# Optimization experiments

Hardware: AMD Instinct MI355X
Metric: run time of the kernel (lower is better)

Reference implementation:

```python
import jax, jax.numpy as jnp
import numpy as np

POOL_D, POOL_H, POOL_W = 4, 7, 7
SPATIAL_SCALE = 0.25
SAMPLING_RATIO = 2


def setup_inputs() -> dict:
    key = jax.random.key(0)
    k1, k2, k3, k4 = jax.random.split(key, 4)
    N, C, D, H, W = 2, 128, 32, 64, 64
    features = jax.random.normal(k1, (N, C, D, H, W), dtype=jnp.float32)
    R = 256
    inv = 1.0 / SPATIAL_SCALE  # rois live in image coords; features at stride 4
    batch = jax.random.randint(k2, (R,), 0, N).astype(jnp.float32)
    dims = jnp.array([D, H, W], dtype=jnp.float32)
    starts = jax.random.uniform(k3, (R, 3)) * dims * inv * 0.6
    sizes = (0.1 + 0.3 * jax.random.uniform(k4, (R, 3))) * dims * inv
    z1, y1, x1 = starts[:, 0], starts[:, 1], starts[:, 2]
    z2, y2, x2 = z1 + sizes[:, 0], y1 + sizes[:, 1], x1 + sizes[:, 2]
    # roi layout: (batch_idx, x1, y1, z1, x2, y2, z2)
    rois = jnp.stack([batch, x1, y1, z1, x2, y2, z2], axis=1).astype(jnp.float32)
    return {"features": features, "rois": rois}


def _axis(coords, size):
    # classic RoIAlign border handling: outside [-1, size] -> 0 contribution
    valid = (coords >= -1.0) & (coords <= float(size))
    c = jnp.clip(coords, 0.0, float(size) - 1.0)
    lo = jnp.floor(c)
    hi = jnp.minimum(lo + 1.0, float(size) - 1.0)
    w = c - lo  # weight of the hi corner
    return lo.astype(jnp.int32), hi.astype(jnp.int32), w, valid


def roi_align_3d(features, rois):
    N, C, D, H, W = features.shape
    R = rois.shape[0]
    sr = SAMPLING_RATIO
    b = rois[:, 0].astype(jnp.int32)
    x1 = rois[:, 1] * SPATIAL_SCALE
    y1 = rois[:, 2] * SPATIAL_SCALE
    z1 = rois[:, 3] * SPATIAL_SCALE
    x2 = rois[:, 4] * SPATIAL_SCALE
    y2 = rois[:, 5] * SPATIAL_SCALE
    z2 = rois[:, 6] * SPATIAL_SCALE
    rd = jnp.maximum(z2 - z1, 1.0)
    rh = jnp.maximum(y2 - y1, 1.0)
    rw = jnp.maximum(x2 - x1, 1.0)

    def sample_coords(start, extent, P):
        # sampling_ratio sample centers per output bin -> [R, P*sr]
        t = (jnp.arange(P * sr, dtype=jnp.float32) + 0.5) / sr
        return start[:, None] + t[None, :] * (extent / P)[:, None]

    zs = sample_coords(z1, rd, POOL_D)  # [R, SD]
    ys = sample_coords(y1, rh, POOL_H)  # [R, SH]
    xs = sample_coords(x1, rw, POOL_W)  # [R, SW]
    zlo, zhi, wz, vz = _axis(zs, D)
    ylo, yhi, wy, vy = _axis(ys, H)
    xlo, xhi, wx, vx = _axis(xs, W)

    B = b[:, None, None, None]
    Z = lambda a: a[:, :, None, None]
    Y = lambda a: a[:, None, :, None]
    X = lambda a: a[:, None, None, :]

    def g(zi, yi, xi):
        # gather -> [R, SD, SH, SW, C]
        return features[B, :, Z(zi), Y(yi), X(xi)]

    wz1, wy1, wx1 = Z(wz)[..., None], Y(wy)[..., None], X(wx)[..., None]
    wz0, wy0, wx0 = 1.0 - wz1, 1.0 - wy1, 1.0 - wx1
    val = (g(zlo, ylo, xlo) * (wz0 * wy0 * wx0)
           + g(zlo, ylo, xhi) * (wz0 * wy0 * wx1)
           + g(zlo, yhi, xlo) * (wz0 * wy1 * wx0)
           + g(zlo, yhi, xhi) * (wz0 * wy1 * wx1)
           + g(zhi, ylo, xlo) * (wz1 * wy0 * wx0)
           + g(zhi, ylo, xhi) * (wz1 * wy0 * wx1)
           + g(zhi, yhi, xlo) * (wz1 * wy1 * wx0)
           + g(zhi, yhi, xhi) * (wz1 * wy1 * wx1))
    valid = (Z(vz) & Y(vy) & X(vx))[..., None]
    val = jnp.where(valid, val, 0.0)
    # average the sr^3 samples per bin
    val = val.reshape(R, POOL_D, sr, POOL_H, sr, POOL_W, sr, C)
    out = val.mean(axis=(2, 4, 6))  # [R, PD, PH, PW, C]
    return jnp.transpose(out, (0, 4, 1, 2, 3))  # [R, C, PD, PH, PW]


def reference(features, rois):
    return roi_align_3d(features, rois)
```

## Files before the change

kernel.cpp:

```cpp
#include <hip/hip_runtime.h>

constexpr int C_  = 128;
constexpr int D_  = 32;
constexpr int H_  = 64;
constexpr int W_  = 64;
constexpr int PD = 4;
constexpr int PH = 7;
constexpr int PW = 7;
constexpr int SR = 2;
constexpr float SCALE = 0.25f;
constexpr int S_ = D_ * H_ * W_;
constexpr int BINS_PER_ROI = PD * PH * PW;
constexpr int SLAB = PH * PW;

typedef float vf4 __attribute__((ext_vector_type(4)));

__device__ __forceinline__ void axis2(float start, float extent, int P, int p,
                                      int size, int lo[2], int hi[2],
                                      float w[2], bool v[2]) {
    float bin = extent / (float)P;
#pragma unroll
    for (int u = 0; u < 2; ++u) {
        float t = ((float)(p * SR + u) + 0.5f) / (float)SR;
        float coord = start + t * bin;
        v[u] = (coord >= -1.0f) && (coord <= (float)size);
        float cc = fminf(fmaxf(coord, 0.0f), (float)size - 1.0f);
        float fl = floorf(cc);
        lo[u] = (int)fl;
        hi[u] = min(lo[u] + 1, size - 1);
        w[u] = cc - fl;
    }
}

struct AxisW {
    int base;
    float w[4];
};

__device__ __forceinline__ AxisW axis_merge(float start, float extent, int P,
                                            int p, int size) {
    const float bin = extent / (float)P;
    const float t0 = ((float)(p * SR) + 0.5f) / (float)SR;
    const float c0 = start + t0 * bin;
    const float va = (c0 >= -1.0f && c0 <= (float)size) ? 1.0f : 0.0f;
    const float cc0 = fminf(fmaxf(c0, 0.0f), (float)size - 1.0f);
    const float fl0 = floorf(cc0);
    const int lo0 = (int)fl0;
    const int hi0 = min(lo0 + 1, size - 1);
    const float f0 = cc0 - fl0;
    const float a0 = (1.0f - f0) * va;
    const float a1 = f0 * va;
    const float t1 = ((float)(p * SR + 1) + 0.5f) / (float)SR;
    const float c1 = start + t1 * bin;
    const float vb = (c1 >= -1.0f && c1 <= (float)size) ? 1.0f : 0.0f;
    const float cc1 = fminf(fmaxf(c1, 0.0f), (float)size - 1.0f);
    const float fl1 = floorf(cc1);
    const int lo1 = (int)fl1;
    const int hi1 = min(lo1 + 1, size - 1);
    const float f1 = cc1 - fl1;
    const float b0 = (1.0f - f1) * vb;
    const float b1 = f1 * vb;

    const int dh0 = hi0 - lo0;
    const int dl1 = lo1 - lo0;
    const int dh1 = hi1 - lo0;

    float w0 = a0, w1 = 0.f, w2 = 0.f, w3 = 0.f;
    if (dh0 == 0) w0 += a1; else w1 += a1;
    w0 += (dl1 == 0) ? b0 : 0.f;
    w1 += (dl1 == 1) ? b0 : 0.f;
    w2 += (dl1 == 2) ? b0 : 0.f;
    w0 += (dh1 == 0) ? b1 : 0.f;
    w1 += (dh1 == 1) ? b1 : 0.f;
    w2 += (dh1 == 2) ? b1 : 0.f;
    w3 += (dh1 == 3) ? b1 : 0.f;

    AxisW r;
    r.base = lo0;
    r.w[0] = w0; r.w[1] = w1; r.w[2] = w2; r.w[3] = w3;
    return r;
}

__device__ __forceinline__ unsigned int f2bf(float f) {
    unsigned int u = __float_as_uint(f);
    u += 0x7fffu + ((u >> 16) & 1u);
    return u >> 16;
}

__device__ __forceinline__ float4 bf4(uint2 v) {
    float4 f;
    f.x = __uint_as_float(v.x << 16);
    f.y = __uint_as_float(v.x & 0xffff0000u);
    f.z = __uint_as_float(v.y << 16);
    f.w = __uint_as_float(v.y & 0xffff0000u);
    return f;
}

__global__ __launch_bounds__(512) void transpose_bf16(
    const float* __restrict__ in, unsigned int* __restrict__ outp) {
    __shared__ unsigned int tileu[256][64];
    const int n  = blockIdx.y;
    const int s0 = blockIdx.x * 256;
    const int t  = threadIdx.x;

    const float* src = in + (size_t)n * C_ * S_;
    unsigned int* dst = outp + (size_t)n * (C_ / 2) * S_;

    {
        const int sl  = t & 63;
        const int cp0 = t >> 6;
#pragma unroll
        for (int p = 0; p < 8; ++p) {
            const int cp = cp0 + 8 * p;
            const int c = cp * 2;
            const vf4 a = __builtin_nontemporal_load(
                (const vf4*)&src[(size_t)c * S_ + (s0 + 4 * sl)]);
            const vf4 b = __builtin_nontemporal_load(
                (const vf4*)&src[(size_t)(c + 1) * S_ + (s0 + 4 * sl)]);
            const int col = cp ^ (sl & 31);
            tileu[4 * sl + 0][col] = f2bf(a.x) | (f2bf(b.x) << 16);
            tileu[4 * sl + 1][col] = f2bf(a.y) | (f2bf(b.y) << 16);
            tileu[4 * sl + 2][col] = f2bf(a.z) | (f2bf(b.z) << 16);
            tileu[4 * sl + 3][col] = f2bf(a.w) | (f2bf(b.w) << 16);
        }
    }
    __syncthreads();
    {
        const int cp2   = (t & 31) * 2;
        const int rbase = t >> 5;
#pragma unroll
        for (int it = 0; it < 16; ++it) {
            const int s = rbase + 16 * it;
            const int w = (s >> 2) & 31;
            uint2 v;
            v.x = tileu[s][cp2 ^ w];
            v.y = tileu[s][(cp2 + 1) ^ w];
            *(uint2*)&dst[(size_t)(s0 + s) * (C_ / 2) + cp2] = v;
        }
    }
}

__global__ __launch_bounds__(512) void roi_align_slab(
    const unsigned short* __restrict__ ft,
    const float* __restrict__ rois,
    float* __restrict__ out,
    int R) {
    __shared__ __align__(16) float tile[SLAB][132];

    int r, pd;
    if ((R & 7) == 0) {
        const int xcd = blockIdx.x & 7;
        const int q = blockIdx.x >> 3;
        pd = q & 3;
        r = ((q >> 2) << 3) + xcd;
    } else {
        r = blockIdx.x >> 2;
        pd = blockIdx.x & 3;
    }

    const int t = threadIdx.x;
    const int grp = t >> 5;
    const int c4 = (t & 31) * 4;

    const float* roi = rois + (size_t)r * 7;
    const int b = (int)roi[0];
    const float x1 = roi[1] * SCALE, y1 = roi[2] * SCALE, z1 = roi[3] * SCALE;
    const float x2 = roi[4] * SCALE, y2 = roi[5] * SCALE, z2 = roi[6] * SCALE;
    const float rd = fmaxf(z2 - z1, 1.0f);
    const float rh = fmaxf(y2 - y1, 1.0f);
    const float rw = fmaxf(x2 - x1, 1.0f);

    AxisW az = axis_merge(z1, rd, PD, pd, D_);
    {
        const float s = 1.0f / (SR * SR * SR);
        az.w[0] *= s; az.w[1] *= s; az.w[2] *= s; az.w[3] *= s;
    }

#pragma unroll 1
    for (int k = 0; k < 4; ++k) {
        const int slot = grp + 16 * k;
        if (slot < SLAB) {
            const int ph = slot / PW;
            const int pw = slot - ph * PW;

            const AxisW ay = axis_merge(y1, rh, PH, ph, H_);
            const AxisW ax = axis_merge(x1, rw, PW, pw, W_);

            float4 acc = make_float4(0.f, 0.f, 0.f, 0.f);
            const unsigned bz = (unsigned)b * D_ + (unsigned)az.base;
#pragma unroll
            for (int iz = 0; iz < 4; ++iz) {
                const float wzv = az.w[iz];
                if (wzv == 0.0f) continue;
                const unsigned rz = (bz + iz) * H_ + (unsigned)ay.base;
#pragma unroll
                for (int iy = 0; iy < 4; ++iy) {
                    const float wyv = ay.w[iy];
                    if (wyv == 0.0f) continue;
                    const float wzy = wzv * wyv;
                    const unsigned rowoff =
                        ((rz + iy) * W_ + (unsigned)ax.base) * C_ + c4;
                    const unsigned short* rowp = ft + rowoff;
#pragma unroll
                    for (int ix = 0; ix < 4; ++ix) {
                        const float wxv = ax.w[ix];
                        if (wxv == 0.0f) continue;
                        const float4 f =
                            bf4(*(const uint2*)(rowp + ix * C_));
                        const float w = wzy * wxv;
                        acc.x += w * f.x;
                        acc.y += w * f.y;
                        acc.z += w * f.z;
                        acc.w += w * f.w;
                    }
                }
            }
            *(float4*)&tile[slot][c4] = acc;
        }
    }

    __syncthreads();

    const size_t obase = (size_t)r * C_ * BINS_PER_ROI + (size_t)pd * SLAB;
#pragma unroll 1
    for (int idx = t; idx < C_ * SLAB; idx += 512) {
        const int c = idx / SLAB;
        const int o = idx - c * SLAB;
        __builtin_nontemporal_store(tile[o][c],
                                    &out[obase + (size_t)c * BINS_PER_ROI + o]);
    }
}

__global__ void roi_align_direct(const float* __restrict__ feat,
                                 const float* __restrict__ rois,
                                 float* __restrict__ out, int total) {
    const int tid = blockIdx.x * blockDim.x + threadIdx.x;
    if (tid >= total) return;
    int t = tid;
    const int pw = t % PW; t /= PW;
    const int ph = t % PH; t /= PH;
    const int pd = t % PD; t /= PD;
    const int c = t % C_;  t /= C_;
    const int r = t;

    const float* roi = rois + (size_t)r * 7;
    const int b = (int)roi[0];
    const float x1 = roi[1] * SCALE, y1 = roi[2] * SCALE, z1 = roi[3] * SCALE;
    const float x2 = roi[4] * SCALE, y2 = roi[5] * SCALE, z2 = roi[6] * SCALE;
    const float rd = fmaxf(z2 - z1, 1.0f);
    const float rh = fmaxf(y2 - y1, 1.0f);
    const float rw = fmaxf(x2 - x1, 1.0f);

    int zlo[2], zhi[2], ylo[2], yhi[2], xlo[2], xhi[2];
    float wz[2], wy[2], wx[2];
    bool vz[2], vy[2], vx[2];
    axis2(z1, rd, PD, pd, D_, zlo, zhi, wz, vz);
    axis2(y1, rh, PH, ph, H_, ylo, yhi, wy, vy);
    axis2(x1, rw, PW, pw, W_, xlo, xhi, wx, vx);

    const float* fc = feat + ((size_t)b * C_ + c) * S_;
    float acc = 0.0f;
#pragma unroll
    for (int i = 0; i < 2; ++i) {
        if (!vz[i]) continue;
#pragma unroll
        for (int j = 0; j < 2; ++j) {
            if (!vy[j]) continue;
            const size_t r00 = ((size_t)zlo[i] * H_ + ylo[j]) * W_;
            const size_t r10 = ((size_t)zhi[i] * H_ + ylo[j]) * W_;
            const size_t r01 = ((size_t)zlo[i] * H_ + yhi[j]) * W_;
            const size_t r11 = ((size_t)zhi[i] * H_ + yhi[j]) * W_;
            const float wz1 = wz[i], wz0 = 1.0f - wz1;
            const float wy1 = wy[j], wy0 = 1.0f - wy1;
#pragma unroll
            for (int k = 0; k < 2; ++k) {
                if (!vx[k]) continue;
                const float wx1 = wx[k], wx0 = 1.0f - wx1;
                acc += wz0 * (wy0 * (wx0 * fc[r00 + xlo[k]] + wx1 * fc[r00 + xhi[k]]) +
                              wy1 * (wx0 * fc[r01 + xlo[k]] + wx1 * fc[r01 + xhi[k]])) +
                       wz1 * (wy0 * (wx0 * fc[r10 + xlo[k]] + wx1 * fc[r10 + xhi[k]]) +
                              wy1 * (wx0 * fc[r11 + xlo[k]] + wx1 * fc[r11 + xhi[k]]));
            }
        }
    }
    out[tid] = acc * (1.0f / (SR * SR * SR));
}

extern "C" void kernel_launch(void* const* d_in, const int* in_sizes, int n_in,
                              void* d_out, int out_size, void* d_ws,
                              size_t ws_size, hipStream_t stream) {
    const float* features = (const float*)d_in[0];
    const float* rois = (const float*)d_in[1];
    float* out = (float*)d_out;

    const int R = in_sizes[1] / 7;
    const int N = in_sizes[0] / (C_ * S_);
    const size_t need = (size_t)in_sizes[0] * sizeof(unsigned short);

    if (ws_size >= need) {
        unsigned short* ft = (unsigned short*)d_ws;

        dim3 tg(S_ / 256, N);
        transpose_bf16<<<tg, 512, 0, stream>>>(features, (unsigned int*)ft);

        roi_align_slab<<<R * PD, 512, 0, stream>>>(ft, rois, out, R);
    } else {
        const int total = R * C_ * BINS_PER_ROI;
        roi_align_direct<<<(total + 255) / 256, 256, 0, stream>>>(
            features, rois, out, total);
    }
}
```

Baseline: 278.6 us.

## Split RoI align into one wave per output bin with lane-parallel x corners

The slab kernel is replaced by a kernel that launches 28 blocks per RoI, one per depth slice and group of 8 bins. Each wave handles a single bin. Its 64 lanes cover 4 x-offsets × 16 channel groups, each lane loading 8 bf16 channels as one 16-byte load, and the partial sums are combined with cross-lane shuffles. This removes the zero-weight branches and gives far more blocks to parallelise the gather. The cost is redundant loads of unweighted corners, a padding zero region at the end of the workspace for x overreads, and more blocks each with a small output write.

After: 254.1 us. -8.8%, faster.

```diff
diff --git a/kernel.cpp b/kernel.cpp
--- a/kernel.cpp
+++ b/kernel.cpp
@@ -87,15 +87,6 @@
     return u >> 16;
 }
 
-__device__ __forceinline__ float4 bf4(uint2 v) {
-    float4 f;
-    f.x = __uint_as_float(v.x << 16);
-    f.y = __uint_as_float(v.x & 0xffff0000u);
-    f.z = __uint_as_float(v.y << 16);
-    f.w = __uint_as_float(v.y & 0xffff0000u);
-    return f;
-}
-
 __global__ __launch_bounds__(512) void transpose_bf16(
     const float* __restrict__ in, unsigned int* __restrict__ outp) {
     __shared__ unsigned int tileu[256][64];
@@ -105,6 +96,10 @@
 
     const float* src = in + (size_t)n * C_ * S_;
     unsigned int* dst = outp + (size_t)n * (C_ / 2) * S_;
+
+    if (n == 0 && blockIdx.x == 0 && t < 256) {
+        outp[(size_t)gridDim.y * (C_ / 2) * S_ + t] = 0u;
+    }
 
     {
         const int sl  = t & 63;
@@ -140,32 +135,40 @@
     }
 }
 
-__global__ __launch_bounds__(512) void roi_align_slab(
+__global__ __launch_bounds__(512) void roi_align_slot(
     const unsigned short* __restrict__ ft,
     const float* __restrict__ rois,
     float* __restrict__ out,
     int R) {
-    __shared__ __align__(16) float tile[SLAB][132];
-
-    int r, pd;
-    if ((R & 7) == 0) {
-        const int xcd = blockIdx.x & 7;
-        const int q = blockIdx.x >> 3;
-        pd = q & 3;
-        r = ((q >> 2) << 3) + xcd;
-    } else {
-        r = blockIdx.x >> 2;
-        pd = blockIdx.x & 3;
+    __shared__ float tile[8][128];
+
+    int roi, pd, part;
+    {
+        const int B = blockIdx.x;
+        if ((R & 7) == 0) {
+            const int xcd = B & 7;
+            const int j = B >> 3;
+            roi = xcd + 8 * (j / 28);
+            const int sub = j % 28;
+            pd = sub / 7;
+            part = sub - pd * 7;
+        } else {
+            roi = B / 28;
+            const int sub = B - roi * 28;
+            pd = sub / 7;
+            part = sub - pd * 7;
+        }
     }
 
     const int t = threadIdx.x;
-    const int grp = t >> 5;
-    const int c4 = (t & 31) * 4;
-
-    const float* roi = rois + (size_t)r * 7;
-    const int b = (int)roi[0];
-    const float x1 = roi[1] * SCALE, y1 = roi[2] * SCALE, z1 = roi[3] * SCALE;
-    const float x2 = roi[4] * SCALE, y2 = roi[5] * SCALE, z2 = roi[6] * SCALE;
+    const int w = t >> 6;
+    const int lane = t & 63;
+    const int slot = part * 8 + w;
+
+    const float* roip = rois + (size_t)roi * 7;
+    const int b = (int)roip[0];
+    const float x1 = roip[1] * SCALE, y1 = roip[2] * SCALE, z1 = roip[3] * SCALE;
+    const float x2 = roip[4] * SCALE, y2 = roip[5] * SCALE, z2 = roip[6] * SCALE;
     const float rd = fmaxf(z2 - z1, 1.0f);
     const float rh = fmaxf(y2 - y1, 1.0f);
     const float rw = fmaxf(x2 - x1, 1.0f);
@@ -176,58 +179,81 @@
         az.w[0] *= s; az.w[1] *= s; az.w[2] *= s; az.w[3] *= s;
     }
 
-#pragma unroll 1
-    for (int k = 0; k < 4; ++k) {
-        const int slot = grp + 16 * k;
-        if (slot < SLAB) {
-            const int ph = slot / PW;
-            const int pw = slot - ph * PW;
-
-            const AxisW ay = axis_merge(y1, rh, PH, ph, H_);
-            const AxisW ax = axis_merge(x1, rw, PW, pw, W_);
-
-            float4 acc = make_float4(0.f, 0.f, 0.f, 0.f);
-            const unsigned bz = (unsigned)b * D_ + (unsigned)az.base;
-#pragma unroll
-            for (int iz = 0; iz < 4; ++iz) {
-                const float wzv = az.w[iz];
-                if (wzv == 0.0f) continue;
-                const unsigned rz = (bz + iz) * H_ + (unsigned)ay.base;
-#pragma unroll
-                for (int iy = 0; iy < 4; ++iy) {
-                    const float wyv = ay.w[iy];
-                    if (wyv == 0.0f) continue;
-                    const float wzy = wzv * wyv;
-                    const unsigned rowoff =
-                        ((rz + iy) * W_ + (unsigned)ax.base) * C_ + c4;
-                    const unsigned short* rowp = ft + rowoff;
-#pragma unroll
-                    for (int ix = 0; ix < 4; ++ix) {
-                        const float wxv = ax.w[ix];
-                        if (wxv == 0.0f) continue;
-                        const float4 f =
-                            bf4(*(const uint2*)(rowp + ix * C_));
-                        const float w = wzy * wxv;
-                        acc.x += w * f.x;
-                        acc.y += w * f.y;
-                        acc.z += w * f.z;
-                        acc.w += w * f.w;
-                    }
-                }
+    if (slot < SLAB) {
+        const int ph = slot / PW;
+        const int pw = slot - ph * PW;
+
+        const AxisW ay = axis_merge(y1, rh, PH, ph, H_);
+        const AxisW ax = axis_merge(x1, rw, PW, pw, W_);
+
+        const int v = lane >> 4;
+        float wxl = ax.w[0];
+        wxl = (v == 1) ? ax.w[1] : wxl;
+        wxl = (v == 2) ? ax.w[2] : wxl;
+        wxl = (v == 3) ? ax.w[3] : wxl;
+
+        float acc[8];
+#pragma unroll
+        for (int j = 0; j < 8; ++j) acc[j] = 0.f;
+
+        const unsigned short* lanep = ft + (unsigned)lane * 8;
+
+#pragma unroll
+        for (int iz = 0; iz < 4; ++iz) {
+            const int zz = min(az.base + iz, D_ - 1);
+            const unsigned zrow = ((unsigned)b * D_ + (unsigned)zz) * H_;
+            const float wzv = az.w[iz];
+#pragma unroll
+            for (int iy = 0; iy < 4; ++iy) {
+                const int yy = min(ay.base + iy, H_ - 1);
+                const float wf = (wzv * ay.w[iy]) * wxl;
+                const unsigned rowe =
+                    ((zrow + (unsigned)yy) * W_ + (unsigned)ax.base) * C_;
+                const uint4 q = *(const uint4*)(lanep + rowe);
+                acc[0] += wf * __uint_as_float(q.x << 16);
+                acc[1] += wf * __uint_as_float(q.x & 0xffff0000u);
+                acc[2] += wf * __uint_as_float(q.y << 16);
+                acc[3] += wf * __uint_as_float(q.y & 0xffff0000u);
+                acc[4] += wf * __uint_as_float(q.z << 16);
+                acc[5] += wf * __uint_as_float(q.z & 0xffff0000u);
+                acc[6] += wf * __uint_as_float(q.w << 16);
+                acc[7] += wf * __uint_as_float(q.w & 0xffff0000u);
             }
-            *(float4*)&tile[slot][c4] = acc;
+        }
+
+#pragma unroll
+        for (int j = 0; j < 8; ++j) {
+            float s = acc[j];
+            s += __shfl_xor(s, 16);
+            s += __shfl_xor(s, 32);
+            acc[j] = s;
+        }
+        if (lane < 16) {
+#pragma unroll
+            for (int j = 0; j < 8; ++j) tile[w][lane * 8 + j] = acc[j];
         }
     }
 
     __syncthreads();
 
-    const size_t obase = (size_t)r * C_ * BINS_PER_ROI + (size_t)pd * SLAB;
-#pragma unroll 1
-    for (int idx = t; idx < C_ * SLAB; idx += 512) {
-        const int c = idx / SLAB;
-        const int o = idx - c * SLAB;
-        __builtin_nontemporal_store(tile[o][c],
-                                    &out[obase + (size_t)c * BINS_PER_ROI + o]);
+    const int s0 = part * 8;
+    const int nslot = SLAB - s0;
+    const size_t obase =
+        (size_t)roi * C_ * BINS_PER_ROI + (size_t)pd * SLAB + s0;
+    if (nslot >= 8) {
+#pragma unroll
+        for (int it = 0; it < 2; ++it) {
+            const int idx = t + it * 512;
+            const int c = idx >> 3;
+            const int o = idx & 7;
+            __builtin_nontemporal_store(
+                tile[o][c], &out[obase + (size_t)c * BINS_PER_ROI + o]);
+        }
+    } else {
+        if (t < C_) {
+            __builtin_nontemporal_store(tile[0][t],
+                                        &out[obase + (size_t)t * BINS_PER_ROI]);
+        }
     }
 }
 
@@ -295,7 +321,7 @@
 
     const int R = in_sizes[1] / 7;
     const int N = in_sizes[0] / (C_ * S_);
-    const size_t need = (size_t)in_sizes[0] * sizeof(unsigned short);
+    const size_t need = (size_t)in_sizes[0] * sizeof(unsigned short) + 1024;
 
     if (ws_size >= need) {
         unsigned short* ft = (unsigned short*)d_ws;
@@ -303,7 +329,7 @@
         dim3 tg(S_ / 256, N);
         transpose_bf16<<<tg, 512, 0, stream>>>(features, (unsigned int*)ft);
 
-        roi_align_slab<<<R * PD, 512, 0, stream>>>(ft, rois, out, R);
+        roi_align_slot<<<R * PD * 7, 512, 0, stream>>>(ft, rois, out, R);
     } else {
         const int total = R * C_ * BINS_PER_ROI;
         roi_align_direct<<<(total + 255) / 256, 256, 0, stream>>>(
```
